# Kernel tuning notes

Hardware: AMD Instinct MI355X
Metric: run time of the kernel (lower is better)

Reference implementation:

```python
import jax, jax.numpy as jnp
import numpy as np

BN_EPS = 1e-5

def setup_inputs() -> dict:
    key = jax.random.key(0)
    ks = jax.random.split(key, 7)
    B, D, A = 16384, 768, 51
    s = 1.0 / np.sqrt(D)
    return {
        "x": jax.random.normal(ks[0], (B, D), dtype=jnp.float32),
        "W_embed": jax.random.uniform(ks[1], (D, D), minval=-s, maxval=s, dtype=jnp.float32),
        "b_embed": jax.random.uniform(ks[2], (D,), minval=-s, maxval=s, dtype=jnp.float32),
        "W_attr": jax.random.uniform(ks[3], (A, D), minval=-s, maxval=s, dtype=jnp.float32),  # stacked per-attribute (dim->1) heads
        "b_attr": jax.random.uniform(ks[4], (A,), minval=-s, maxval=s, dtype=jnp.float32),
        "gamma": jnp.ones((A,), dtype=jnp.float32),
        "beta": jnp.zeros((A,), dtype=jnp.float32),
    }

def reference(x, W_embed, b_embed, W_attr, b_attr, gamma, beta):
    # word_embed: Linear(dim, dim)
    h = x @ W_embed.T + b_embed                      # [B, D]
    # fused per-attribute heads: cat of attr_num (dim->1) linears == one (dim->attr_num) matmul
    logits = h @ W_attr.T + b_attr                    # [B, A]
    # BatchNorm1d (training mode: batch statistics, biased variance)
    mean = jnp.mean(logits, axis=0)
    var = jnp.var(logits, axis=0)
    y = (logits - mean) * jax.lax.rsqrt(var + BN_EPS) * gamma + beta
    return y
```

## Files before the change

kernel.cpp:

```cpp
#include <hip/hip_runtime.h>

typedef _Float16 halfx8 __attribute__((ext_vector_type(8)));
typedef float floatx4 __attribute__((ext_vector_type(4)));

#define GLOBAL_AS __attribute__((address_space(1)))
#define LDS_AS __attribute__((address_space(3)))

__device__ __forceinline__ void async_copy_16(const void* g, void* l) {
    __builtin_amdgcn_global_load_lds((GLOBAL_AS void*)g, (LDS_AS void*)l, 16, 0, 0);
}

#define PM 16384
#define PD 768
#define PA 51
#define NBLK 256u


__global__ __launch_bounds__(256) void prep_kernel(
    const float* __restrict__ We, const float* __restrict__ be,
    const float* __restrict__ Wa, const float* __restrict__ ba,
    _Float16* __restrict__ wc16, float* __restrict__ bc, float* __restrict__ stats,
    unsigned int* __restrict__ counter)
{
    const int wave = threadIdx.x >> 6;
    const int lane = threadIdx.x & 63;
    const int Wu = __builtin_amdgcn_readfirstlane((int)blockIdx.x * 4 + wave);

    if (Wu < 312) {
        const int pair = Wu / 12;
        const int dchunk = Wu - pair * 12;
        const int a0 = pair * 2;
        const bool has1 = (a0 + 1 < PA);
        const int d = dchunk * 64 + lane;
        const float* wa0 = Wa + (size_t)a0 * PD;
        const float* wa1 = Wa + (size_t)(has1 ? a0 + 1 : a0) * PD;
        float acc0 = 0.f, acc1 = 0.f;
        #pragma unroll 32
        for (int k = 0; k < PD; ++k) {
            float w = We[(size_t)k * PD + d];
            acc0 = fmaf(w, wa0[k], acc0);
            acc1 = fmaf(w, wa1[k], acc1);
        }
        wc16[(size_t)a0 * PD + d] = (_Float16)acc0;
        if (has1) wc16[(size_t)(a0 + 1) * PD + d] = (_Float16)acc1;
    } else if (Wu < 325) {
        const int r = PA + (Wu - 312);
        #pragma unroll
        for (int j = 0; j < 12; ++j)
            wc16[(size_t)r * PD + j * 64 + lane] = (_Float16)0.f;
    } else if (Wu < 376) {
        const int a = Wu - 325;
        float p = 0.f;
        #pragma unroll
        for (int j = 0; j < 12; ++j) {
            int k = j * 64 + lane;
            p = fmaf(Wa[(size_t)a * PD + k], be[k], p);
        }
        #pragma unroll
        for (int off = 32; off; off >>= 1) p += __shfl_down(p, off);
        if (lane == 0) bc[a] = p + ba[a];
    } else if (Wu == 376) {
        stats[lane] = 0.f;
        stats[64 + lane] = 0.f;
        if (lane == 0) *counter = 0u;
    }
}

__global__ void __launch_bounds__(512, 1) gemm_bn_kernel(
    const float* __restrict__ X,
    const _Float16* __restrict__ Wc16,
    const float* __restrict__ bc,
    const float* __restrict__ gamma,
    const float* __restrict__ beta,
    float* __restrict__ out,
    float* __restrict__ stats,
    unsigned int* __restrict__ counter)
{
    __shared__ __attribute__((aligned(16))) float As[3][64 * 64];
    __shared__ __attribute__((aligned(16))) _Float16 Bh[64 * PD];
    __shared__ float s_sum[64];
    __shared__ float s_ssq[64];

    const int tid = threadIdx.x;
    const int wave = tid >> 6;
    const int lane = tid & 63;
    const int quad = lane >> 4;
    const int l16 = lane & 15;
    const int wr = wave & 3;
    const int wn = wave >> 2;
    const int row0 = (int)blockIdx.x * 64;

    if (tid < 64) { s_sum[tid] = 0.f; s_ssq[tid] = 0.f; }

    #pragma unroll
    for (int j = 0; j < 12; ++j) {
        int gc = (wave * 12 + j) * 64 + lane;
        int r = gc / 96;
        int c = gc - r * 96;
        int csw = (c & ~7) | ((c & 7) ^ (r & 7));
        async_copy_16(Wc16 + (size_t)r * PD + csw * 8,
                      (char*)Bh + (size_t)(wave * 12 + j) * 1024);
    }
    asm volatile("" ::: "memory");

    auto stageA = [&](int buf, int kt) {
        #pragma unroll
        for (int j = 0; j < 2; ++j) {
            int chunkbase = (wave * 2 + j) * 64;
            int chunk = chunkbase + lane;
            int r = chunk >> 4;
            int c = chunk & 15;
            int csw = (c & 8) | ((c & 7) ^ (r & 7));
            async_copy_16(X + (size_t)(row0 + r) * PD + kt + csw * 4,
                          (char*)&As[buf][0] + (size_t)chunkbase * 16);
        }
        asm volatile("" ::: "memory");
    };

    floatx4 acc[2];
    acc[0] = (floatx4){0.f, 0.f, 0.f, 0.f};
    acc[1] = (floatx4){0.f, 0.f, 0.f, 0.f};

    auto computeT = [&](int t, const float* AsB) {
        #pragma unroll
        for (int ks = 0; ks < 2; ++ks) {
            int c0 = ks * 8 + quad * 2;
            int sw = l16 & 7;
            int rA = wr * 16 + l16;
            floatx4 p0 = *(const floatx4*)&AsB[rA * 64 + ((c0 ^ sw) << 2)];
            floatx4 p1 = *(const floatx4*)&AsB[rA * 64 + (((c0 + 1) ^ sw) << 2)];
            halfx8 af;
            af[0] = (_Float16)p0[0]; af[1] = (_Float16)p0[1];
            af[2] = (_Float16)p0[2]; af[3] = (_Float16)p0[3];
            af[4] = (_Float16)p1[0]; af[5] = (_Float16)p1[1];
            af[6] = (_Float16)p1[2]; af[7] = (_Float16)p1[3];
            #pragma unroll
            for (int ni = 0; ni < 2; ++ni) {
                int rB = wn * 32 + ni * 16 + l16;
                int hc = t * 8 + (((ks * 4 + quad)) ^ (rB & 7));
                halfx8 bf = *(const halfx8*)&Bh[(size_t)rB * PD + (hc << 3)];
                acc[ni] = __builtin_amdgcn_mfma_f32_16x16x32_f16(af, bf, acc[ni], 0, 0, 0);
            }
        }
    };

    stageA(0, 0);
    stageA(1, 64);
    stageA(2, 128);
    #pragma unroll
    for (int t = 0; t < 12; ++t) {
        if (t <= 9)       asm volatile("s_waitcnt vmcnt(4)\n\ts_barrier" ::: "memory");
        else if (t == 10) asm volatile("s_waitcnt vmcnt(2)\n\ts_barrier" ::: "memory");
        else              asm volatile("s_waitcnt vmcnt(0)\n\ts_barrier" ::: "memory");
        computeT(t, &As[t % 3][0]);
        asm volatile("s_waitcnt lgkmcnt(0)\n\ts_barrier" ::: "memory");
        if (t + 3 < 12) stageA(t % 3, (t + 3) * 64);
    }

    float keep[2][4];
    int cols[2];
    #pragma unroll
    for (int ni = 0; ni < 2; ++ni) {
        int col = wn * 32 + ni * 16 + l16;
        cols[ni] = col;
        if (col < PA) {
            float bv = bc[col];
            float ps = 0.f, pss = 0.f;
            #pragma unroll
            for (int r = 0; r < 4; ++r) {
                float v = acc[ni][r] + bv;
                keep[ni][r] = v;
                ps += v; pss += v * v;
            }
            atomicAdd(&s_sum[col], ps);
            atomicAdd(&s_ssq[col], pss);
        }
    }
    __syncthreads();
    if (tid < PA) {
        atomicAdd(&stats[tid], s_sum[tid]);
        atomicAdd(&stats[64 + tid], s_ssq[tid]);
    }
    __syncthreads();

    if (tid == 0) {
        __hip_atomic_fetch_add(counter, 1u, __ATOMIC_ACQ_REL, __HIP_MEMORY_SCOPE_AGENT);
        while (__hip_atomic_load(counter, __ATOMIC_ACQUIRE, __HIP_MEMORY_SCOPE_AGENT) < NBLK)
            __builtin_amdgcn_s_sleep(8);
    }
    __syncthreads();

    const float invB = 1.0f / (float)PM;
    #pragma unroll
    for (int ni = 0; ni < 2; ++ni) {
        int col = cols[ni];
        if (col < PA) {
            float s  = __hip_atomic_load(&stats[col],      __ATOMIC_RELAXED, __HIP_MEMORY_SCOPE_AGENT);
            float ss = __hip_atomic_load(&stats[64 + col], __ATOMIC_RELAXED, __HIP_MEMORY_SCOPE_AGENT);
            float mean = s * invB;
            float var  = ss * invB - mean * mean;
            float inv  = rsqrtf(var + 1e-5f);
            float scale = gamma[col] * inv;
            float shift = beta[col] - mean * scale;
            int rowb = row0 + wr * 16 + quad * 4;
            #pragma unroll
            for (int r = 0; r < 4; ++r)
                out[(size_t)(rowb + r) * PA + col] = keep[ni][r] * scale + shift;
        }
    }
}

extern "C" void kernel_launch(void* const* d_in, const int* in_sizes, int n_in,
                              void* d_out, int out_size, void* d_ws, size_t ws_size,
                              hipStream_t stream) {
    const float* x       = (const float*)d_in[0];
    const float* W_embed = (const float*)d_in[1];
    const float* b_embed = (const float*)d_in[2];
    const float* W_attr  = (const float*)d_in[3];
    const float* b_attr  = (const float*)d_in[4];
    const float* gamma   = (const float*)d_in[5];
    const float* beta    = (const float*)d_in[6];
    float* out = (float*)d_out;

    char* ws = (char*)d_ws;
    _Float16* wc16        = (_Float16*)(ws);
    float* bc             = (float*)(ws + 98304);
    float* stats          = (float*)(ws + 98816);
    unsigned int* counter = (unsigned int*)(ws + 99584);

    prep_kernel<<<95, 256, 0, stream>>>(W_embed, b_embed, W_attr, b_attr,
                                        wc16, bc, stats, counter);
    gemm_bn_kernel<<<256, 512, 0, stream>>>(x, wc16, bc, gamma, beta, out,
                                            stats, counter);
}
```

Before: 151.5 us.

## Prelayout fused weight in MFMA fragment order and give each wave private A tiles

The prep kernel now writes the fused fp16 weight directly in MFMA B-fragment order, so the GEMM kernel loads it into LDS with plain linear copies and reads each fragment with one contiguous access per lane. The GEMM block drops from 8 to 4 waves. Each wave owns a 16-row strip and all 64 output columns, with its own triple-buffered A tiles. This removes the block-wide barriers in the K loop. It trades half as many waves per block and more accumulators per wave for no cross-wave synchronisation during the main loop.

```diff
diff --git a/kernel.cpp b/kernel.cpp
--- a/kernel.cpp
+++ b/kernel.cpp
@@ -16,10 +16,15 @@
 #define NBLK 256u
 
 
+__device__ __forceinline__ size_t fragidx(int a, int d) {
+    return (size_t)(d >> 5) * 2048 + (size_t)(a >> 4) * 512
+         + (size_t)((a & 15) | (((d >> 3) & 3) << 4)) * 8 + (d & 7);
+}
+
 __global__ __launch_bounds__(256) void prep_kernel(
     const float* __restrict__ We, const float* __restrict__ be,
     const float* __restrict__ Wa, const float* __restrict__ ba,
-    _Float16* __restrict__ wc16, float* __restrict__ bc, float* __restrict__ stats,
+    _Float16* __restrict__ wfrag, float* __restrict__ bc, float* __restrict__ stats,
     unsigned int* __restrict__ counter)
 {
     const int wave = threadIdx.x >> 6;
@@ -41,13 +46,13 @@
             acc0 = fmaf(w, wa0[k], acc0);
             acc1 = fmaf(w, wa1[k], acc1);
         }
-        wc16[(size_t)a0 * PD + d] = (_Float16)acc0;
-        if (has1) wc16[(size_t)(a0 + 1) * PD + d] = (_Float16)acc1;
+        wfrag[fragidx(a0, d)] = (_Float16)acc0;
+        if (has1) wfrag[fragidx(a0 + 1, d)] = (_Float16)acc1;
     } else if (Wu < 325) {
         const int r = PA + (Wu - 312);
         #pragma unroll
         for (int j = 0; j < 12; ++j)
-            wc16[(size_t)r * PD + j * 64 + lane] = (_Float16)0.f;
+            wfrag[fragidx(r, j * 64 + lane)] = (_Float16)0.f;
     } else if (Wu < 376) {
         const int a = Wu - 325;
         float p = 0.f;
@@ -66,9 +71,9 @@
     }
 }
 
-__global__ void __launch_bounds__(512, 1) gemm_bn_kernel(
+__global__ void __launch_bounds__(256, 1) gemm_bn_kernel(
     const float* __restrict__ X,
-    const _Float16* __restrict__ Wc16,
+    const _Float16* __restrict__ Wfrag,
     const float* __restrict__ bc,
     const float* __restrict__ gamma,
     const float* __restrict__ beta,
@@ -76,8 +81,8 @@
     float* __restrict__ stats,
     unsigned int* __restrict__ counter)
 {
-    __shared__ __attribute__((aligned(16))) float As[3][64 * 64];
-    __shared__ __attribute__((aligned(16))) _Float16 Bh[64 * PD];
+    __shared__ __attribute__((aligned(16))) _Float16 Bh[24 * 4 * 512];
+    __shared__ __attribute__((aligned(16))) float Atile[4][3][16 * 64];
     __shared__ float s_sum[64];
     __shared__ float s_ssq[64];
 
@@ -86,90 +91,77 @@
     const int lane = tid & 63;
     const int quad = lane >> 4;
     const int l16 = lane & 15;
-    const int wr = wave & 3;
-    const int wn = wave >> 2;
-    const int row0 = (int)blockIdx.x * 64;
+    const int m0 = (int)blockIdx.x * 64 + wave * 16;
 
     if (tid < 64) { s_sum[tid] = 0.f; s_ssq[tid] = 0.f; }
 
     #pragma unroll
-    for (int j = 0; j < 12; ++j) {
-        int gc = (wave * 12 + j) * 64 + lane;
-        int r = gc / 96;
-        int c = gc - r * 96;
-        int csw = (c & ~7) | ((c & 7) ^ (r & 7));
-        async_copy_16(Wc16 + (size_t)r * PD + csw * 8,
-                      (char*)Bh + (size_t)(wave * 12 + j) * 1024);
+    for (int j = 0; j < 24; ++j) {
+        int ch = wave * 24 + j;
+        async_copy_16((const char*)Wfrag + (size_t)ch * 1024 + (size_t)lane * 16,
+                      (char*)Bh + (size_t)ch * 1024);
     }
     asm volatile("" ::: "memory");
 
     auto stageA = [&](int buf, int kt) {
         #pragma unroll
-        for (int j = 0; j < 2; ++j) {
-            int chunkbase = (wave * 2 + j) * 64;
-            int chunk = chunkbase + lane;
-            int r = chunk >> 4;
-            int c = chunk & 15;
+        for (int j = 0; j < 4; ++j) {
+            int r = j * 4 + (lane >> 4);
+            int c = lane & 15;
             int csw = (c & 8) | ((c & 7) ^ (r & 7));
-            async_copy_16(X + (size_t)(row0 + r) * PD + kt + csw * 4,
-                          (char*)&As[buf][0] + (size_t)chunkbase * 16);
+            async_copy_16(X + (size_t)(m0 + r) * PD + kt + csw * 4,
+                          (char*)&Atile[wave][buf][0] + (size_t)(j * 64) * 16);
         }
         asm volatile("" ::: "memory");
     };
 
-    floatx4 acc[2];
-    acc[0] = (floatx4){0.f, 0.f, 0.f, 0.f};
-    acc[1] = (floatx4){0.f, 0.f, 0.f, 0.f};
-
-    auto computeT = [&](int t, const float* AsB) {
-        #pragma unroll
-        for (int ks = 0; ks < 2; ++ks) {
-            int c0 = ks * 8 + quad * 2;
-            int sw = l16 & 7;
-            int rA = wr * 16 + l16;
-            floatx4 p0 = *(const floatx4*)&AsB[rA * 64 + ((c0 ^ sw) << 2)];
-            floatx4 p1 = *(const floatx4*)&AsB[rA * 64 + (((c0 + 1) ^ sw) << 2)];
+    floatx4 acc[4];
+    #pragma unroll
+    for (int n = 0; n < 4; ++n) acc[n] = (floatx4){0.f, 0.f, 0.f, 0.f};
+
+    stageA(0, 0);
+    stageA(1, 64);
+    stageA(2, 128);
+    asm volatile("s_waitcnt vmcnt(12)\n\ts_barrier" ::: "memory");
+
+    #pragma unroll
+    for (int mm = 0; mm < 12; ++mm) {
+        if (mm <= 9)       asm volatile("s_waitcnt vmcnt(8)" ::: "memory");
+        else if (mm == 10) asm volatile("s_waitcnt vmcnt(4)" ::: "memory");
+        else               asm volatile("s_waitcnt vmcnt(0)" ::: "memory");
+        const float* At = &Atile[wave][mm % 3][0];
+        #pragma unroll
+        for (int km = 0; km < 2; ++km) {
+            const int ks = mm * 2 + km;
+            int cc = km * 8 + quad * 2;
+            int s3 = l16 & 7;
+            floatx4 p0 = *(const floatx4*)&At[l16 * 64 + (((cc & 8) | ((cc & 7) ^ s3)) << 2)];
+            floatx4 p1 = *(const floatx4*)&At[l16 * 64 + ((((cc + 1) & 8) | (((cc + 1) & 7) ^ s3)) << 2)];
             halfx8 af;
             af[0] = (_Float16)p0[0]; af[1] = (_Float16)p0[1];
             af[2] = (_Float16)p0[2]; af[3] = (_Float16)p0[3];
             af[4] = (_Float16)p1[0]; af[5] = (_Float16)p1[1];
             af[6] = (_Float16)p1[2]; af[7] = (_Float16)p1[3];
             #pragma unroll
-            for (int ni = 0; ni < 2; ++ni) {
-                int rB = wn * 32 + ni * 16 + l16;
-                int hc = t * 8 + (((ks * 4 + quad)) ^ (rB & 7));
-                halfx8 bf = *(const halfx8*)&Bh[(size_t)rB * PD + (hc << 3)];
-                acc[ni] = __builtin_amdgcn_mfma_f32_16x16x32_f16(af, bf, acc[ni], 0, 0, 0);
+            for (int n = 0; n < 4; ++n) {
+                halfx8 bf = *(const halfx8*)&Bh[(size_t)(ks * 4 + n) * 512 + (size_t)lane * 8];
+                acc[n] = __builtin_amdgcn_mfma_f32_16x16x32_f16(af, bf, acc[n], 0, 0, 0);
             }
         }
-    };
-
-    stageA(0, 0);
-    stageA(1, 64);
-    stageA(2, 128);
-    #pragma unroll
-    for (int t = 0; t < 12; ++t) {
-        if (t <= 9)       asm volatile("s_waitcnt vmcnt(4)\n\ts_barrier" ::: "memory");
-        else if (t == 10) asm volatile("s_waitcnt vmcnt(2)\n\ts_barrier" ::: "memory");
-        else              asm volatile("s_waitcnt vmcnt(0)\n\ts_barrier" ::: "memory");
-        computeT(t, &As[t % 3][0]);
-        asm volatile("s_waitcnt lgkmcnt(0)\n\ts_barrier" ::: "memory");
-        if (t + 3 < 12) stageA(t % 3, (t + 3) * 64);
-    }
-
-    float keep[2][4];
-    int cols[2];
-    #pragma unroll
-    for (int ni = 0; ni < 2; ++ni) {
-        int col = wn * 32 + ni * 16 + l16;
-        cols[ni] = col;
+        if (mm + 3 < 12) stageA(mm % 3, (mm + 3) * 64);
+    }
+
+    float keep[4][4];
+    #pragma unroll
+    for (int n = 0; n < 4; ++n) {
+        int col = n * 16 + l16;
         if (col < PA) {
             float bv = bc[col];
             float ps = 0.f, pss = 0.f;
             #pragma unroll
             for (int r = 0; r < 4; ++r) {
-                float v = acc[ni][r] + bv;
-                keep[ni][r] = v;
+                float v = acc[n][r] + bv;
+                keep[n][r] = v;
                 ps += v; pss += v * v;
             }
             atomicAdd(&s_sum[col], ps);
@@ -185,15 +177,16 @@
 
     if (tid == 0) {
         __hip_atomic_fetch_add(counter, 1u, __ATOMIC_ACQ_REL, __HIP_MEMORY_SCOPE_AGENT);
-        while (__hip_atomic_load(counter, __ATOMIC_ACQUIRE, __HIP_MEMORY_SCOPE_AGENT) < NBLK)
+        while (__hip_atomic_load(counter, __ATOMIC_RELAXED, __HIP_MEMORY_SCOPE_AGENT) < NBLK)
             __builtin_amdgcn_s_sleep(8);
+        (void)__hip_atomic_load(counter, __ATOMIC_ACQUIRE, __HIP_MEMORY_SCOPE_AGENT);
     }
     __syncthreads();
 
     const float invB = 1.0f / (float)PM;
     #pragma unroll
-    for (int ni = 0; ni < 2; ++ni) {
-        int col = cols[ni];
+    for (int n = 0; n < 4; ++n) {
+        int col = n * 16 + l16;
         if (col < PA) {
             float s  = __hip_atomic_load(&stats[col],      __ATOMIC_RELAXED, __HIP_MEMORY_SCOPE_AGENT);
             float ss = __hip_atomic_load(&stats[64 + col], __ATOMIC_RELAXED, __HIP_MEMORY_SCOPE_AGENT);
@@ -202,10 +195,10 @@
             float inv  = rsqrtf(var + 1e-5f);
             float scale = gamma[col] * inv;
             float shift = beta[col] - mean * scale;
-            int rowb = row0 + wr * 16 + quad * 4;
+            int rowb = m0 + quad * 4;
             #pragma unroll
             for (int r = 0; r < 4; ++r)
-                out[(size_t)(rowb + r) * PA + col] = keep[ni][r] * scale + shift;
+                out[(size_t)(rowb + r) * PA + col] = keep[n][r] * scale + shift;
         }
     }
 }
@@ -223,13 +216,13 @@
     float* out = (float*)d_out;
 
     char* ws = (char*)d_ws;
-    _Float16* wc16        = (_Float16*)(ws);
+    _Float16* wfrag       = (_Float16*)(ws);
     float* bc             = (float*)(ws + 98304);
     float* stats          = (float*)(ws + 98816);
     unsigned int* counter = (unsigned int*)(ws + 99584);
 
     prep_kernel<<<95, 256, 0, stream>>>(W_embed, b_embed, W_attr, b_attr,
-                                        wc16, bc, stats, counter);
-    gemm_bn_kernel<<<256, 512, 0, stream>>>(x, wc16, bc, gamma, beta, out,
+                                        wfrag, bc, stats, counter);
+    gemm_bn_kernel<<<256, 256, 0, stream>>>(x, wfrag, bc, gamma, beta, out,
                                             stats, counter);
 }
```

Measured after the change: 147.1 us. 2.9% less time.
